# Kernel optimization log

Hardware: AMD Instinct MI355X
Metric: run time of the kernel (lower is better)

The kernel has to match this reference:

```python
import jax, jax.numpy as jnp
import numpy as np

EPS_DIST = 1e-8
EPS_BN = 1e-5


def _bn_relu(x, g, b):
    # training-mode BatchNorm1d over (batch, spatial) per channel, then ReLU
    mean = jnp.mean(x, axis=(0, 2), keepdims=True)
    var = jnp.mean((x - mean) ** 2, axis=(0, 2), keepdims=True)
    xhat = (x - mean) * jax.lax.rsqrt(var + EPS_BN)
    return jax.nn.relu(xhat * g[None, :, None] + b[None, :, None])


def setup_inputs() -> dict:
    key = jax.random.key(0)
    ks = jax.random.split(key, 8)
    B, N, M, C1, C2 = 8, 16384, 4096, 64, 256
    return {
        "p1": jax.random.normal(ks[0], (B, N, 3), jnp.float32),
        "p2": jax.random.normal(ks[1], (B, M, 3), jnp.float32),
        "f1": jax.random.normal(ks[2], (B, C1, N), jnp.float32),
        "f2": jax.random.normal(ks[3], (B, C2, M), jnp.float32),
        "idx": jax.random.randint(ks[4], (B, N, 3), 0, M, jnp.int64),
        "W1": jax.random.normal(ks[5], (256, C1 + C2), jnp.float32) * 0.05,
        "g1": jnp.ones((256,), jnp.float32),
        "b1": jnp.zeros((256,), jnp.float32),
        "W2": jax.random.normal(ks[6], (256, 256), jnp.float32) * 0.05,
        "g2": jnp.ones((256,), jnp.float32),
        "b2": jnp.zeros((256,), jnp.float32),
    }


def reference(p1, p2, f1, f2, idx, W1, g1, b1, W2, g2, b2):
    B = p1.shape[0]
    b_ix = jnp.arange(B)[:, None, None]  # batch index for gathers
    # --- three_interpolation: inverse-squared-distance weighted 3-NN interp ---
    nbr_xyz = p2[b_ix, idx]                     # [B, N, 3, 3]
    d2 = jnp.sum((p1[:, :, None, :] - nbr_xyz) ** 2, axis=-1)  # [B, N, 3]
    recip = 1.0 / (d2 + EPS_DIST)
    weight = recip / jnp.sum(recip, axis=-1, keepdims=True)    # [B, N, 3]
    f2_nbr = jnp.swapaxes(f2, 1, 2)[b_ix, idx]  # [B, N, 3, C2]
    interp = jnp.einsum("bnkc,bnk->bcn", f2_nbr, weight)       # [B, C2, N]
    # --- concat + two 1x1 conv + BN + ReLU blocks ---
    x = jnp.concatenate((f1, interp), axis=1)   # [B, C1+C2, N]
    x = _bn_relu(jnp.einsum("oi,bin->bon", W1, x), g1, b1)
    x = _bn_relu(jnp.einsum("oi,bin->bon", W2, x), g2, b2)
    return x
```

## Files before the change

kernel.cpp:

```cpp
#include <hip/hip_runtime.h>
#include <hip/hip_bf16.h>

#define BB 8
#define NN 16384
#define MM 4096
#define C1 64
#define C2 256
#define K1 320
#define CO 256
#define MTOT (BB * NN)

#define STATS_OFF 0
#define FLAG_OFF  8192
#define W1B_OFF   16384
#define W2B_OFF   180224
#define F2T_OFF   327680
#define XT_OFF    (327680 + 16777216)
#define H2_OFF    (327680 + 16777216 + 83886080)


typedef short v8s __attribute__((ext_vector_type(8)));
typedef float v4f __attribute__((ext_vector_type(4)));

__device__ __forceinline__ float bf2f(unsigned short u) {
    unsigned v = ((unsigned)u) << 16;
    float f;
    __builtin_memcpy(&f, &v, 4);
    return f;
}
__device__ __forceinline__ unsigned short f2bf(float f) {
    unsigned u;
    __builtin_memcpy(&u, &f, 4);
    unsigned r = u + 0x7fffu + ((u >> 16) & 1u);
    return (unsigned short)(r >> 16);
}
__device__ __forceinline__ void gload16(const unsigned short* g, unsigned short* l) {
    __builtin_amdgcn_global_load_lds((const __attribute__((address_space(1))) unsigned int*)g,
                                     (__attribute__((address_space(3))) unsigned int*)l, 16, 0, 0);
}

__global__ void k_prep(const void* idx_raw, int* flag64, float* stats,
                       const float* __restrict__ W1, unsigned short* __restrict__ W1b,
                       const float* __restrict__ W2, unsigned short* __restrict__ W2b) {
    int blk = blockIdx.x;
    int t = threadIdx.x;
    if (blk < 320) {
        int e = blk * 256 + t;
        int row = e / K1, col = e - row * K1;
        W1b[row * K1 + (col ^ ((row & 7) << 3))] = f2bf(W1[e]);
    } else if (blk < 576) {
        int e = (blk - 320) * 256 + t;
        int row = e >> 8, col = e & 255;
        W2b[row * CO + (col ^ ((row & 7) << 3))] = f2bf(W2[e]);
    } else {
        for (int i = t; i < 8 * 256; i += 256) stats[i] = 0.f;
        if (t == 0) {
            const int* a = (const int*)idx_raw;
            int all0 = 1;
            for (int j = 1; j < 64; j += 2) all0 &= (a[j] == 0);
            *flag64 = all0;
        }
    }
}

__global__ void k_tr_f2(const float* __restrict__ f2, unsigned short* __restrict__ f2t) {
    __shared__ float tile[64][33];
    int b = blockIdx.z;
    int c0 = blockIdx.y * 64;
    int m0 = blockIdx.x * 32;
    int t = threadIdx.x;
    int lm = t & 31, lc = t >> 5;
    const float* src = f2 + ((size_t)b * C2 + c0) * MM + m0;
#pragma unroll
    for (int j = 0; j < 8; ++j)
        tile[lc + 8 * j][lm] = src[(size_t)(lc + 8 * j) * MM + lm];
    __syncthreads();
    int m = t >> 3, c8 = (t & 7) * 8;
    unsigned short tmp[8];
#pragma unroll
    for (int k = 0; k < 8; ++k) tmp[k] = f2bf(tile[c8 + k][m]);
    uint4 v;
    v.x = (unsigned)tmp[0] | ((unsigned)tmp[1] << 16);
    v.y = (unsigned)tmp[2] | ((unsigned)tmp[3] << 16);
    v.z = (unsigned)tmp[4] | ((unsigned)tmp[5] << 16);
    v.w = (unsigned)tmp[6] | ((unsigned)tmp[7] << 16);
    *(uint4*)&f2t[((size_t)b * MM + m0 + m) * C2 + c0 + c8] = v;
}

__global__ void k_tr_f1(const float* __restrict__ f1, unsigned short* __restrict__ xT) {
    __shared__ float tile[64][33];
    int b = blockIdx.z;
    int n0 = blockIdx.x * 32;
    int t = threadIdx.x;
    int lm = t & 31, lc = t >> 5;
    const float* src = f1 + ((size_t)b * C1) * NN + n0;
#pragma unroll
    for (int j = 0; j < 8; ++j)
        tile[lc + 8 * j][lm] = src[(size_t)(lc + 8 * j) * NN + lm];
    __syncthreads();
    int m = t >> 3, c8 = (t & 7) * 8;
    unsigned short tmp[8];
#pragma unroll
    for (int k = 0; k < 8; ++k) tmp[k] = f2bf(tile[c8 + k][m]);
    uint4 v;
    v.x = (unsigned)tmp[0] | ((unsigned)tmp[1] << 16);
    v.y = (unsigned)tmp[2] | ((unsigned)tmp[3] << 16);
    v.z = (unsigned)tmp[4] | ((unsigned)tmp[5] << 16);
    v.w = (unsigned)tmp[6] | ((unsigned)tmp[7] << 16);
    *(uint4*)&xT[((size_t)b * NN + n0 + m) * K1 + (c8 ^ ((m & 7) * 8))] = v;
}

__global__ void k_interp(const float* __restrict__ p1, const float* __restrict__ p2,
                         const void* __restrict__ idxv, const int* __restrict__ flag64,
                         const unsigned short* __restrict__ f2t,
                         unsigned short* __restrict__ xT) {
    int t = threadIdx.x;
    int p = t >> 5, lane = t & 31;
    size_t pt = (size_t)blockIdx.x * 8 + p;
    int b = (int)(pt >> 14);
    int m0, m1, m2;
    if (*flag64) {
        const long long* id = (const long long*)idxv;
        m0 = (int)id[pt * 3 + 0]; m1 = (int)id[pt * 3 + 1]; m2 = (int)id[pt * 3 + 2];
    } else {
        const int* id = (const int*)idxv;
        m0 = id[pt * 3 + 0]; m1 = id[pt * 3 + 1]; m2 = id[pt * 3 + 2];
    }
    float qx = p1[pt * 3 + 0], qy = p1[pt * 3 + 1], qz = p1[pt * 3 + 2];
    const float* pb = p2 + (size_t)b * MM * 3;
    float dx, dy, dz;
    dx = qx - pb[m0 * 3 + 0]; dy = qy - pb[m0 * 3 + 1]; dz = qz - pb[m0 * 3 + 2];
    float d0 = dx * dx + dy * dy + dz * dz;
    dx = qx - pb[m1 * 3 + 0]; dy = qy - pb[m1 * 3 + 1]; dz = qz - pb[m1 * 3 + 2];
    float d1 = dx * dx + dy * dy + dz * dz;
    dx = qx - pb[m2 * 3 + 0]; dy = qy - pb[m2 * 3 + 1]; dz = qz - pb[m2 * 3 + 2];
    float d2v = dx * dx + dy * dy + dz * dz;
    float r0 = 1.f / (d0 + 1e-8f), r1 = 1.f / (d1 + 1e-8f), r2 = 1.f / (d2v + 1e-8f);
    float inv = 1.f / (r0 + r1 + r2);
    float w0 = r0 * inv, w1 = r1 * inv, w2 = r2 * inv;

    const unsigned short* fb = f2t + (size_t)b * MM * C2;
    int c0 = lane * 8;
    uint4 va = *(const uint4*)(fb + (size_t)m0 * C2 + c0);
    uint4 vb = *(const uint4*)(fb + (size_t)m1 * C2 + c0);
    uint4 vc = *(const uint4*)(fb + (size_t)m2 * C2 + c0);

    float r[8];
    {
        const unsigned av[4] = {va.x, va.y, va.z, va.w};
        const unsigned bv[4] = {vb.x, vb.y, vb.z, vb.w};
        const unsigned cv[4] = {vc.x, vc.y, vc.z, vc.w};
#pragma unroll
        for (int q = 0; q < 4; ++q) {
            r[2 * q + 0] = w0 * bf2f((unsigned short)(av[q] & 0xffff))
                         + w1 * bf2f((unsigned short)(bv[q] & 0xffff))
                         + w2 * bf2f((unsigned short)(cv[q] & 0xffff));
            r[2 * q + 1] = w0 * bf2f((unsigned short)(av[q] >> 16))
                         + w1 * bf2f((unsigned short)(bv[q] >> 16))
                         + w2 * bf2f((unsigned short)(cv[q] >> 16));
        }
    }
    uint4 outv;
    outv.x = (unsigned)f2bf(r[0]) | ((unsigned)f2bf(r[1]) << 16);
    outv.y = (unsigned)f2bf(r[2]) | ((unsigned)f2bf(r[3]) << 16);
    outv.z = (unsigned)f2bf(r[4]) | ((unsigned)f2bf(r[5]) << 16);
    outv.w = (unsigned)f2bf(r[6]) | ((unsigned)f2bf(r[7]) << 16);
    *(uint4*)(xT + pt * K1 + ((C1 + c0) ^ (((int)pt & 7) * 8))) = outv;
}

#define TM 128
#define TN 128
#define TK 64
__launch_bounds__(256)
__global__ void k_gemm1(const unsigned short* __restrict__ xT,
                        const unsigned short* __restrict__ W1b,
                        unsigned short* __restrict__ h1,
                        float* __restrict__ sum1, float* __restrict__ ssq1) {
    __shared__ unsigned short smem[2][TM * TK + TN * TK];
    const int t = threadIdx.x;
    const int lane = t & 63, w = t >> 6;
    const int wm = w >> 1, wc = w & 1;
    const long rbase = (long)blockIdx.y * TM;
    const int cb = blockIdx.x * TN;

    v4f acc[4][4];
#pragma unroll
    for (int r = 0; r < 4; ++r)
#pragma unroll
        for (int c = 0; c < 4; ++c) acc[r][c] = (v4f)(0.f);

    const int srow = w * 32 + (lane >> 3);
    const int sch = (lane & 7) * 8;
    const unsigned short* Ag = xT + (rbase + srow) * K1 + sch;
    const unsigned short* Bg = W1b + (size_t)(cb + srow) * K1 + sch;

    const int ln = lane & 15, q = lane >> 4;
    const int xs = (ln & 7) * 8;

#pragma unroll
    for (int j = 0; j < 4; ++j) {
        gload16(Ag + (size_t)(j * 8) * K1, smem[0] + (w * 32 + j * 8) * TK);
        gload16(Bg + (size_t)(j * 8) * K1, smem[0] + TM * TK + (w * 32 + j * 8) * TK);
    }
    __syncthreads();

    for (int k0 = 0; k0 < K1; k0 += TK) {
        const int p = (k0 >> 6) & 1;
        if (k0 + TK < K1) {
#pragma unroll
            for (int j = 0; j < 4; ++j) {
                gload16(Ag + (size_t)(j * 8) * K1 + k0 + TK, smem[p ^ 1] + (w * 32 + j * 8) * TK);
                gload16(Bg + (size_t)(j * 8) * K1 + k0 + TK, smem[p ^ 1] + TM * TK + (w * 32 + j * 8) * TK);
            }
        }
        const unsigned short* ApL = smem[p] + (wm * 64 + ln) * TK;
        const unsigned short* BpL = smem[p] + TM * TK + (wc * 64 + ln) * TK;
#pragma unroll
        for (int ks = 0; ks < 2; ++ks) {
            const int off = (q * 8 + ks * 32) ^ xs;
            v8s af[4], bg[4];
#pragma unroll
            for (int r = 0; r < 4; ++r) af[r] = *(const v8s*)(ApL + r * 16 * TK + off);
#pragma unroll
            for (int c = 0; c < 4; ++c) bg[c] = *(const v8s*)(BpL + c * 16 * TK + off);
#pragma unroll
            for (int r = 0; r < 4; ++r)
#pragma unroll
                for (int c = 0; c < 4; ++c)
                    acc[r][c] = __builtin_amdgcn_mfma_f32_16x16x32_bf16(af[r], bg[c], acc[r][c], 0, 0, 0);
        }
        __syncthreads();
    }

    unsigned short* ep = (unsigned short*)smem;
#pragma unroll
    for (int c = 0; c < 4; ++c) {
        int col = wc * 64 + c * 16 + ln;
        int cc = col >> 3, ci = col & 7;
        float s = 0.f, sq = 0.f;
#pragma unroll
        for (int r = 0; r < 4; ++r)
#pragma unroll
            for (int i = 0; i < 4; ++i) {
                int row = wm * 64 + r * 16 + q * 4 + i;
                float v = acc[r][c][i];
                ep[row * 128 + 8 * (cc ^ (row & 15)) + ci] = f2bf(v);
                s += v; sq += v * v;
            }
        s += __shfl_xor(s, 16); sq += __shfl_xor(sq, 16);
        s += __shfl_xor(s, 32); sq += __shfl_xor(sq, 32);
        if (lane < 16) {
            atomicAdd(&sum1[cb + col], s);
            atomicAdd(&ssq1[cb + col], sq);
        }
    }
    __syncthreads();
    {
        int rr = t >> 4, cc2 = t & 15;
#pragma unroll
        for (int j = 0; j < 8; ++j) {
            int row = rr + 16 * j;
            uint4 v = *(const uint4*)&ep[row * 128 + 8 * (cc2 ^ (row & 15))];
            *(uint4*)&h1[(size_t)(rbase + row) * CO + cb + cc2 * 8] = v;
        }
    }
}

__launch_bounds__(256)
__global__ void k_gemm2(const unsigned short* __restrict__ h1,
                        const unsigned short* __restrict__ W2b,
                        const float* __restrict__ sum1, const float* __restrict__ ssq1,
                        const float* __restrict__ g1, const float* __restrict__ b1,
                        unsigned short* __restrict__ h2,
                        float* __restrict__ sum2, float* __restrict__ ssq2) {
    __shared__ unsigned short smem[2][TM * TK + TN * TK];
    __shared__ float sc1[CO], sh1[CO];
    const int t = threadIdx.x;
    const int lane = t & 63, w = t >> 6;
    const int wm = w >> 1, wc = w & 1;
    const long rbase = (long)blockIdx.y * TM;
    const int cb = blockIdx.x * TN;

    {
        const float invn = 1.f / (float)MTOT;
        float m = sum1[t] * invn;
        float v = ssq1[t] * invn - m * m;
        float s = g1[t] * rsqrtf(v + 1e-5f);
        sc1[t] = s;
        sh1[t] = b1[t] - m * s;
    }
    __syncthreads();

    v4f acc[4][4];
#pragma unroll
    for (int r = 0; r < 4; ++r)
#pragma unroll
        for (int c = 0; c < 4; ++c) acc[r][c] = (v4f)(0.f);

    const int srow = w * 32 + (lane >> 3);
    const int sch = (lane & 7) * 8;
    const unsigned short* Ag = h1 + (rbase + srow) * CO + sch;
    const unsigned short* Bg = W2b + (size_t)(cb + srow) * CO + sch;
    const int awz = srow * TK + (sch ^ ((srow & 7) * 8));

    const int ln = lane & 15, q = lane >> 4;
    const int xs = (ln & 7) * 8;

#define CONV_STORE(AV, KOFF, BASE)                                                     \
    do {                                                                               \
        float4 sca = *(const float4*)(sc1 + (KOFF) + sch);                             \
        float4 scb = *(const float4*)(sc1 + (KOFF) + sch + 4);                         \
        float4 sha = *(const float4*)(sh1 + (KOFF) + sch);                             \
        float4 shb = *(const float4*)(sh1 + (KOFF) + sch + 4);                         \
        _Pragma("unroll")                                                              \
        for (int j = 0; j < 4; ++j) {                                                  \
            uint4 av = (AV)[j];                                                        \
            float y0 = fmaxf(bf2f((unsigned short)(av.x & 0xffff)) * sca.x + sha.x, 0.f); \
            float y1 = fmaxf(bf2f((unsigned short)(av.x >> 16)) * sca.y + sha.y, 0.f); \
            float y2 = fmaxf(bf2f((unsigned short)(av.y & 0xffff)) * sca.z + sha.z, 0.f); \
            float y3 = fmaxf(bf2f((unsigned short)(av.y >> 16)) * sca.w + sha.w, 0.f); \
            float y4 = fmaxf(bf2f((unsigned short)(av.z & 0xffff)) * scb.x + shb.x, 0.f); \
            float y5 = fmaxf(bf2f((unsigned short)(av.z >> 16)) * scb.y + shb.y, 0.f); \
            float y6 = fmaxf(bf2f((unsigned short)(av.w & 0xffff)) * scb.z + shb.z, 0.f); \
            float y7 = fmaxf(bf2f((unsigned short)(av.w >> 16)) * scb.w + shb.w, 0.f); \
            uint4 ov;                                                                  \
            ov.x = (unsigned)f2bf(y0) | ((unsigned)f2bf(y1) << 16);                    \
            ov.y = (unsigned)f2bf(y2) | ((unsigned)f2bf(y3) << 16);                    \
            ov.z = (unsigned)f2bf(y4) | ((unsigned)f2bf(y5) << 16);                    \
            ov.w = (unsigned)f2bf(y6) | ((unsigned)f2bf(y7) << 16);                    \
            *(uint4*)((BASE) + awz + (j * 8) * TK) = ov;                               \
        }                                                                              \
    } while (0)

    uint4 avc[4], avn[4];
#pragma unroll
    for (int j = 0; j < 4; ++j)
        gload16(Bg + (size_t)(j * 8) * CO, smem[0] + TM * TK + (w * 32 + j * 8) * TK);
#pragma unroll
    for (int j = 0; j < 4; ++j) avc[j] = *(const uint4*)(Ag + (size_t)(j * 8) * CO);
#pragma unroll
    for (int j = 0; j < 4; ++j) avn[j] = *(const uint4*)(Ag + (size_t)(j * 8) * CO + TK);
    CONV_STORE(avc, 0, smem[0]);
    __syncthreads();

#pragma unroll
    for (int kk = 0; kk < 4; ++kk) {
        const int p = kk & 1;
        if (kk < 3) {
#pragma unroll
            for (int j = 0; j < 4; ++j)
                gload16(Bg + (size_t)(j * 8) * CO + (kk + 1) * TK,
                        smem[p ^ 1] + TM * TK + (w * 32 + j * 8) * TK);
            CONV_STORE(avn, (kk + 1) * TK, smem[p ^ 1]);
        }
        if (kk < 2) {
#pragma unroll
            for (int j = 0; j < 4; ++j)
                avn[j] = *(const uint4*)(Ag + (size_t)(j * 8) * CO + (kk + 2) * TK);
        }
        const unsigned short* ApL = smem[p] + (wm * 64 + ln) * TK;
        const unsigned short* BpL = smem[p] + TM * TK + (wc * 64 + ln) * TK;
#pragma unroll
        for (int ks = 0; ks < 2; ++ks) {
            const int off = (q * 8 + ks * 32) ^ xs;
            v8s af[4], bg4[4];
#pragma unroll
            for (int r = 0; r < 4; ++r) af[r] = *(const v8s*)(ApL + r * 16 * TK + off);
#pragma unroll
            for (int c = 0; c < 4; ++c) bg4[c] = *(const v8s*)(BpL + c * 16 * TK + off);
#pragma unroll
            for (int r = 0; r < 4; ++r)
#pragma unroll
                for (int c = 0; c < 4; ++c)
                    acc[r][c] = __builtin_amdgcn_mfma_f32_16x16x32_bf16(af[r], bg4[c], acc[r][c], 0, 0, 0);
        }
        __syncthreads();
    }
#undef CONV_STORE

    unsigned short* ep = (unsigned short*)smem;
    const int b = (int)(rbase >> 14);
    const int nb = (int)(rbase & (NN - 1));
#pragma unroll
    for (int c = 0; c < 4; ++c) {
        int ol = wc * 64 + c * 16 + ln;
        float s = 0.f, sq = 0.f;
#pragma unroll
        for (int r = 0; r < 4; ++r)
#pragma unroll
            for (int i = 0; i < 4; ++i) {
                int row = wm * 64 + r * 16 + q * 4 + i;
                int rc = row >> 3, ri = row & 7;
                float v = acc[r][c][i];
                ep[ol * 128 + 8 * (rc ^ (ol & 15)) + ri] = f2bf(v);
                s += v; sq += v * v;
            }
        s += __shfl_xor(s, 16); sq += __shfl_xor(sq, 16);
        s += __shfl_xor(s, 32); sq += __shfl_xor(sq, 32);
        if (lane < 16) {
            atomicAdd(&sum2[cb + ol], s);
            atomicAdd(&ssq2[cb + ol], sq);
        }
    }
    __syncthreads();
    {
        int oo = t >> 4, nc = t & 15;
#pragma unroll
        for (int j = 0; j < 8; ++j) {
            int ol = oo + 16 * j;
            uint4 v = *(const uint4*)&ep[ol * 128 + 8 * (nc ^ (ol & 15))];
            *(uint4*)&h2[(((size_t)(b * CO + cb + ol)) << 14) + nb + nc * 8] = v;
        }
    }
}

__global__ void k_apply(const unsigned short* __restrict__ h2,
                        const float* __restrict__ sum2, const float* __restrict__ ssq2,
                        const float* __restrict__ g2, const float* __restrict__ b2,
                        float* __restrict__ out) {
    __shared__ float ss[2];
    int o = (blockIdx.x >> 4) & 255;
    if (threadIdx.x == 0) {
        const float invn = 1.f / (float)MTOT;
        float m = sum2[o] * invn;
        float v = ssq2[o] * invn - m * m;
        float s = g2[o] * rsqrtf(v + 1e-5f);
        ss[0] = s;
        ss[1] = b2[o] - m * s;
    }
    __syncthreads();
    float s = ss[0], d = ss[1];
    size_t i = ((size_t)blockIdx.x * 256 + threadIdx.x) * 4;
    ushort4 hv = *(const ushort4*)(h2 + i);
    float4 v;
    v.x = fmaxf(bf2f(hv.x) * s + d, 0.f);
    v.y = fmaxf(bf2f(hv.y) * s + d, 0.f);
    v.z = fmaxf(bf2f(hv.z) * s + d, 0.f);
    v.w = fmaxf(bf2f(hv.w) * s + d, 0.f);
    *(float4*)&out[i] = v;
}

extern "C" void kernel_launch(void* const* d_in, const int* in_sizes, int n_in,
                              void* d_out, int out_size, void* d_ws, size_t ws_size,
                              hipStream_t stream) {
    const float* p1 = (const float*)d_in[0];
    const float* p2 = (const float*)d_in[1];
    const float* f1 = (const float*)d_in[2];
    const float* f2 = (const float*)d_in[3];
    const void*  idx = d_in[4];
    const float* W1 = (const float*)d_in[5];
    const float* g1 = (const float*)d_in[6];
    const float* b1 = (const float*)d_in[7];
    const float* W2 = (const float*)d_in[8];
    const float* g2 = (const float*)d_in[9];
    const float* b2 = (const float*)d_in[10];
    float* out = (float*)d_out;

    char* ws = (char*)d_ws;
    float* stats = (float*)(ws + STATS_OFF);
    float* sum1 = stats + 0;     float* ssq1 = stats + 256;
    float* sum2 = stats + 1024;  float* ssq2 = stats + 1280;
    int* flag64 = (int*)(ws + FLAG_OFF);
    unsigned short* W1b = (unsigned short*)(ws + W1B_OFF);
    unsigned short* W2b = (unsigned short*)(ws + W2B_OFF);
    unsigned short* f2t = (unsigned short*)(ws + F2T_OFF);
    unsigned short* xT  = (unsigned short*)(ws + XT_OFF);
    unsigned short* h2  = (unsigned short*)(ws + H2_OFF);

    unsigned short* h1 = (unsigned short*)d_out;

    k_prep<<<577, 256, 0, stream>>>(idx, flag64, stats, W1, W1b, W2, W2b);
    k_tr_f2<<<dim3(MM / 32, C2 / 64, BB), 256, 0, stream>>>(f2, f2t);
    k_tr_f1<<<dim3(NN / 32, 1, BB), 256, 0, stream>>>(f1, xT);
    k_interp<<<MTOT / 8, 256, 0, stream>>>(p1, p2, idx, flag64, f2t, xT);
    k_gemm1<<<dim3(CO / TN, MTOT / TM), 256, 0, stream>>>(xT, W1b, h1, sum1, ssq1);
    k_gemm2<<<dim3(CO / TN, MTOT / TM), 256, 0, stream>>>(h1, W2b, sum1, ssq1, g1, b1, h2, sum2, ssq2);
    k_apply<<<(int)((size_t)out_size / 4 / 256), 256, 0, stream>>>(h2, sum2, ssq2, g2, b2, out);
}
```

Baseline: 404.5 us.

## Merge prep/transpose kernels and single-buffer B tile in GEMMs to cut LDS

Folds the weight-conversion, stats-zeroing and the two transpose kernels into a single launch using block-index ranges, which removes two kernel launches. In both GEMMs the B tile is now single-buffered while A stays double-buffered, reducing LDS per block (from 64KB to 48KB) so more blocks can fit per CU. The cost is an extra barrier and a serialized B reload after each k-step, so B loads no longer overlap with MFMA work.

```diff
diff --git a/kernel.cpp b/kernel.cpp
--- a/kernel.cpp
+++ b/kernel.cpp
@@ -39,9 +39,12 @@
                                      (__attribute__((address_space(3))) unsigned int*)l, 16, 0, 0);
 }
 
-__global__ void k_prep(const void* idx_raw, int* flag64, float* stats,
-                       const float* __restrict__ W1, unsigned short* __restrict__ W1b,
-                       const float* __restrict__ W2, unsigned short* __restrict__ W2b) {
+__global__ void k_pre(const void* idx_raw, int* flag64, float* stats,
+                      const float* __restrict__ W1, unsigned short* __restrict__ W1b,
+                      const float* __restrict__ W2, unsigned short* __restrict__ W2b,
+                      const float* __restrict__ f2, unsigned short* __restrict__ f2t,
+                      const float* __restrict__ f1, unsigned short* __restrict__ xT) {
+    __shared__ float tile[64][33];
     int blk = blockIdx.x;
     int t = threadIdx.x;
     if (blk < 320) {
@@ -52,7 +55,7 @@
         int e = (blk - 320) * 256 + t;
         int row = e >> 8, col = e & 255;
         W2b[row * CO + (col ^ ((row & 7) << 3))] = f2bf(W2[e]);
-    } else {
+    } else if (blk == 576) {
         for (int i = t; i < 8 * 256; i += 256) stats[i] = 0.f;
         if (t == 0) {
             const int* a = (const int*)idx_raw;
@@ -60,54 +63,48 @@
             for (int j = 1; j < 64; j += 2) all0 &= (a[j] == 0);
             *flag64 = all0;
         }
-    }
-}
-
-__global__ void k_tr_f2(const float* __restrict__ f2, unsigned short* __restrict__ f2t) {
-    __shared__ float tile[64][33];
-    int b = blockIdx.z;
-    int c0 = blockIdx.y * 64;
-    int m0 = blockIdx.x * 32;
-    int t = threadIdx.x;
-    int lm = t & 31, lc = t >> 5;
-    const float* src = f2 + ((size_t)b * C2 + c0) * MM + m0;
-#pragma unroll
-    for (int j = 0; j < 8; ++j)
-        tile[lc + 8 * j][lm] = src[(size_t)(lc + 8 * j) * MM + lm];
-    __syncthreads();
-    int m = t >> 3, c8 = (t & 7) * 8;
-    unsigned short tmp[8];
-#pragma unroll
-    for (int k = 0; k < 8; ++k) tmp[k] = f2bf(tile[c8 + k][m]);
-    uint4 v;
-    v.x = (unsigned)tmp[0] | ((unsigned)tmp[1] << 16);
-    v.y = (unsigned)tmp[2] | ((unsigned)tmp[3] << 16);
-    v.z = (unsigned)tmp[4] | ((unsigned)tmp[5] << 16);
-    v.w = (unsigned)tmp[6] | ((unsigned)tmp[7] << 16);
-    *(uint4*)&f2t[((size_t)b * MM + m0 + m) * C2 + c0 + c8] = v;
-}
-
-__global__ void k_tr_f1(const float* __restrict__ f1, unsigned short* __restrict__ xT) {
-    __shared__ float tile[64][33];
-    int b = blockIdx.z;
-    int n0 = blockIdx.x * 32;
-    int t = threadIdx.x;
-    int lm = t & 31, lc = t >> 5;
-    const float* src = f1 + ((size_t)b * C1) * NN + n0;
-#pragma unroll
-    for (int j = 0; j < 8; ++j)
-        tile[lc + 8 * j][lm] = src[(size_t)(lc + 8 * j) * NN + lm];
-    __syncthreads();
-    int m = t >> 3, c8 = (t & 7) * 8;
-    unsigned short tmp[8];
-#pragma unroll
-    for (int k = 0; k < 8; ++k) tmp[k] = f2bf(tile[c8 + k][m]);
-    uint4 v;
-    v.x = (unsigned)tmp[0] | ((unsigned)tmp[1] << 16);
-    v.y = (unsigned)tmp[2] | ((unsigned)tmp[3] << 16);
-    v.z = (unsigned)tmp[4] | ((unsigned)tmp[5] << 16);
-    v.w = (unsigned)tmp[6] | ((unsigned)tmp[7] << 16);
-    *(uint4*)&xT[((size_t)b * NN + n0 + m) * K1 + (c8 ^ ((m & 7) * 8))] = v;
+    } else if (blk < 577 + 4096) {
+        int i = blk - 577;
+        int m0 = (i & 127) * 32;
+        int c0 = ((i >> 7) & 3) * 64;
+        int b = i >> 9;
+        int lm = t & 31, lc = t >> 5;
+        const float* src = f2 + ((size_t)b * C2 + c0) * MM + m0;
+#pragma unroll
+        for (int j = 0; j < 8; ++j)
+            tile[lc + 8 * j][lm] = src[(size_t)(lc + 8 * j) * MM + lm];
+        __syncthreads();
+        int m = t >> 3, c8 = (t & 7) * 8;
+        unsigned short tmp[8];
+#pragma unroll
+        for (int k = 0; k < 8; ++k) tmp[k] = f2bf(tile[c8 + k][m]);
+        uint4 v;
+        v.x = (unsigned)tmp[0] | ((unsigned)tmp[1] << 16);
+        v.y = (unsigned)tmp[2] | ((unsigned)tmp[3] << 16);
+        v.z = (unsigned)tmp[4] | ((unsigned)tmp[5] << 16);
+        v.w = (unsigned)tmp[6] | ((unsigned)tmp[7] << 16);
+        *(uint4*)&f2t[((size_t)b * MM + m0 + m) * C2 + c0 + c8] = v;
+    } else {
+        int i = blk - 4673;
+        int n0 = (i & 511) * 32;
+        int b = i >> 9;
+        int lm = t & 31, lc = t >> 5;
+        const float* src = f1 + ((size_t)b * C1) * NN + n0;
+#pragma unroll
+        for (int j = 0; j < 8; ++j)
+            tile[lc + 8 * j][lm] = src[(size_t)(lc + 8 * j) * NN + lm];
+        __syncthreads();
+        int m = t >> 3, c8 = (t & 7) * 8;
+        unsigned short tmp[8];
+#pragma unroll
+        for (int k = 0; k < 8; ++k) tmp[k] = f2bf(tile[c8 + k][m]);
+        uint4 v;
+        v.x = (unsigned)tmp[0] | ((unsigned)tmp[1] << 16);
+        v.y = (unsigned)tmp[2] | ((unsigned)tmp[3] << 16);
+        v.z = (unsigned)tmp[4] | ((unsigned)tmp[5] << 16);
+        v.w = (unsigned)tmp[6] | ((unsigned)tmp[7] << 16);
+        *(uint4*)&xT[((size_t)b * NN + n0 + m) * K1 + (c8 ^ ((m & 7) * 8))] = v;
+    }
 }
 
 __global__ void k_interp(const float* __restrict__ p1, const float* __restrict__ p2,
@@ -176,7 +173,8 @@
                         const unsigned short* __restrict__ W1b,
                         unsigned short* __restrict__ h1,
                         float* __restrict__ sum1, float* __restrict__ ssq1) {
-    __shared__ unsigned short smem[2][TM * TK + TN * TK];
+    __shared__ unsigned short Ab[2][TM * TK];
+    __shared__ unsigned short Bs[TN * TK];
     const int t = threadIdx.x;
     const int lane = t & 63, w = t >> 6;
     const int wm = w >> 1, wc = w & 1;
@@ -199,22 +197,21 @@
 
 #pragma unroll
     for (int j = 0; j < 4; ++j) {
-        gload16(Ag + (size_t)(j * 8) * K1, smem[0] + (w * 32 + j * 8) * TK);
-        gload16(Bg + (size_t)(j * 8) * K1, smem[0] + TM * TK + (w * 32 + j * 8) * TK);
+        gload16(Ag + (size_t)(j * 8) * K1, Ab[0] + (w * 32 + j * 8) * TK);
+        gload16(Bg + (size_t)(j * 8) * K1, Bs + (w * 32 + j * 8) * TK);
     }
     __syncthreads();
 
     for (int k0 = 0; k0 < K1; k0 += TK) {
         const int p = (k0 >> 6) & 1;
-        if (k0 + TK < K1) {
-#pragma unroll
-            for (int j = 0; j < 4; ++j) {
-                gload16(Ag + (size_t)(j * 8) * K1 + k0 + TK, smem[p ^ 1] + (w * 32 + j * 8) * TK);
-                gload16(Bg + (size_t)(j * 8) * K1 + k0 + TK, smem[p ^ 1] + TM * TK + (w * 32 + j * 8) * TK);
-            }
-        }
-        const unsigned short* ApL = smem[p] + (wm * 64 + ln) * TK;
-        const unsigned short* BpL = smem[p] + TM * TK + (wc * 64 + ln) * TK;
+        const bool notlast = (k0 + TK < K1);
+        if (notlast) {
+#pragma unroll
+            for (int j = 0; j < 4; ++j)
+                gload16(Ag + (size_t)(j * 8) * K1 + k0 + TK, Ab[p ^ 1] + (w * 32 + j * 8) * TK);
+        }
+        const unsigned short* ApL = Ab[p] + (wm * 64 + ln) * TK;
+        const unsigned short* BpL = Bs + (wc * 64 + ln) * TK;
 #pragma unroll
         for (int ks = 0; ks < 2; ++ks) {
             const int off = (q * 8 + ks * 32) ^ xs;
@@ -230,9 +227,15 @@
                     acc[r][c] = __builtin_amdgcn_mfma_f32_16x16x32_bf16(af[r], bg[c], acc[r][c], 0, 0, 0);
         }
         __syncthreads();
-    }
-
-    unsigned short* ep = (unsigned short*)smem;
+        if (notlast) {
+#pragma unroll
+            for (int j = 0; j < 4; ++j)
+                gload16(Bg + (size_t)(j * 8) * K1 + k0 + TK, Bs + (w * 32 + j * 8) * TK);
+            __syncthreads();
+        }
+    }
+
+    unsigned short* ep = &Ab[0][0];
 #pragma unroll
     for (int c = 0; c < 4; ++c) {
         int col = wc * 64 + c * 16 + ln;
@@ -273,7 +276,8 @@
                         const float* __restrict__ g1, const float* __restrict__ b1,
                         unsigned short* __restrict__ h2,
                         float* __restrict__ sum2, float* __restrict__ ssq2) {
-    __shared__ unsigned short smem[2][TM * TK + TN * TK];
+    __shared__ unsigned short Ab[2][TM * TK];
+    __shared__ unsigned short Bs[TN * TK];
     __shared__ float sc1[CO], sh1[CO];
     const int t = threadIdx.x;
     const int lane = t & 63, w = t >> 6;
@@ -289,7 +293,6 @@
         sc1[t] = s;
         sh1[t] = b1[t] - m * s;
     }
-    __syncthreads();
 
     v4f acc[4][4];
 #pragma unroll
@@ -335,31 +338,28 @@
     uint4 avc[4], avn[4];
 #pragma unroll
     for (int j = 0; j < 4; ++j)
-        gload16(Bg + (size_t)(j * 8) * CO, smem[0] + TM * TK + (w * 32 + j * 8) * TK);
+        gload16(Bg + (size_t)(j * 8) * CO, Bs + (w * 32 + j * 8) * TK);
 #pragma unroll
     for (int j = 0; j < 4; ++j) avc[j] = *(const uint4*)(Ag + (size_t)(j * 8) * CO);
 #pragma unroll
     for (int j = 0; j < 4; ++j) avn[j] = *(const uint4*)(Ag + (size_t)(j * 8) * CO + TK);
-    CONV_STORE(avc, 0, smem[0]);
+    __syncthreads();
+    CONV_STORE(avc, 0, Ab[0]);
     __syncthreads();
 
 #pragma unroll
     for (int kk = 0; kk < 4; ++kk) {
         const int p = kk & 1;
         if (kk < 3) {
-#pragma unroll
-            for (int j = 0; j < 4; ++j)
-                gload16(Bg + (size_t)(j * 8) * CO + (kk + 1) * TK,
-                        smem[p ^ 1] + TM * TK + (w * 32 + j * 8) * TK);
-            CONV_STORE(avn, (kk + 1) * TK, smem[p ^ 1]);
+            CONV_STORE(avn, (kk + 1) * TK, Ab[p ^ 1]);
         }
         if (kk < 2) {
 #pragma unroll
             for (int j = 0; j < 4; ++j)
                 avn[j] = *(const uint4*)(Ag + (size_t)(j * 8) * CO + (kk + 2) * TK);
         }
-        const unsigned short* ApL = smem[p] + (wm * 64 + ln) * TK;
-        const unsigned short* BpL = smem[p] + TM * TK + (wc * 64 + ln) * TK;
+        const unsigned short* ApL = Ab[p] + (wm * 64 + ln) * TK;
+        const unsigned short* BpL = Bs + (wc * 64 + ln) * TK;
 #pragma unroll
         for (int ks = 0; ks < 2; ++ks) {
             const int off = (q * 8 + ks * 32) ^ xs;
@@ -375,10 +375,16 @@
                     acc[r][c] = __builtin_amdgcn_mfma_f32_16x16x32_bf16(af[r], bg4[c], acc[r][c], 0, 0, 0);
         }
         __syncthreads();
+        if (kk < 3) {
+#pragma unroll
+            for (int j = 0; j < 4; ++j)
+                gload16(Bg + (size_t)(j * 8) * CO + (kk + 1) * TK, Bs + (w * 32 + j * 8) * TK);
+            __syncthreads();
+        }
     }
 #undef CONV_STORE
 
-    unsigned short* ep = (unsigned short*)smem;
+    unsigned short* ep = &Ab[0][0];
     const int b = (int)(rbase >> 14);
     const int nb = (int)(rbase & (NN - 1));
 #pragma unroll
@@ -469,9 +475,8 @@
 
     unsigned short* h1 = (unsigned short*)d_out;
 
-    k_prep<<<577, 256, 0, stream>>>(idx, flag64, stats, W1, W1b, W2, W2b);
-    k_tr_f2<<<dim3(MM / 32, C2 / 64, BB), 256, 0, stream>>>(f2, f2t);
-    k_tr_f1<<<dim3(NN / 32, 1, BB), 256, 0, stream>>>(f1, xT);
+    k_pre<<<577 + 4096 + 4096, 256, 0, stream>>>(idx, flag64, stats, W1, W1b, W2, W2b,
+                                                 f2, f2t, f1, xT);
     k_interp<<<MTOT / 8, 256, 0, stream>>>(p1, p2, idx, flag64, f2t, xT);
     k_gemm1<<<dim3(CO / TN, MTOT / TM), 256, 0, stream>>>(xT, W1b, h1, sum1, ssq1);
     k_gemm2<<<dim3(CO / TN, MTOT / TM), 256, 0, stream>>>(h1, W2b, sum1, ssq1, g1, b1, h2, sum2, ssq2);
```

Result: no change. 408.6 us (+1.0%).
